# Performance work log

Hardware: AMD Instinct MI355X
Metric: run time of the kernel (lower is better)

## Reference

```python
import jax, jax.numpy as jnp
import numpy as np

N, E, F, H, O, B = 100000, 1200000, 64, 1024, 1, 256


def _gcn_conv(x, W, b, src, dst, ew, num_nodes):
    # PyG GCNConv: out_i = sum_{(s->i)} d_i^{-1/2} w_e d_s^{-1/2} (x_s W) + b
    deg = jax.ops.segment_sum(ew, dst, num_segments=num_nodes)
    dinv = jnp.where(deg > 0, jax.lax.rsqrt(jnp.maximum(deg, 1e-12)), 0.0)
    norm = dinv[src] * ew * dinv[dst]          # [E]
    h = x @ W                                   # [N, out]
    msg = h[src] * norm[:, None]                # gather + scale
    return jax.ops.segment_sum(msg, dst, num_segments=num_nodes) + b


def setup_inputs() -> dict:
    key = jax.random.key(0)
    ks = jax.random.split(key, 12)
    def lin(k, fan_in, fan_out):
        s = 1.0 / np.sqrt(fan_in)
        kw, kb = jax.random.split(k)
        return (jax.random.uniform(kw, (fan_in, fan_out), jnp.float32, -s, s),
                jax.random.uniform(kb, (fan_out,), jnp.float32, -s, s))
    W1, b1 = lin(ks[0], F, F)
    W2, b2 = lin(ks[1], F, 2 * F)
    W3, b3 = lin(ks[2], 2 * F, 4 * F)
    Wf1, bf1 = lin(ks[3], 5 * F, H)
    Wf2, bf2 = lin(ks[4], H, O)
    feature = jax.random.normal(ks[5], (N, F), jnp.float32)
    edge_index = jax.random.randint(ks[6], (2, E), 0, N, jnp.int32)
    weight = jax.random.uniform(ks[7], (E,), jnp.float32)
    protein_batch = jnp.sort(jax.random.randint(ks[8], (N,), 0, B, jnp.int32))
    return {"feature": feature, "edge_index": edge_index, "weight": weight,
            "protein_batch": protein_batch,
            "W1": W1, "b1": b1, "W2": W2, "b2": b2, "W3": W3, "b3": b3,
            "Wf1": Wf1, "bf1": bf1, "Wf2": Wf2, "bf2": bf2}


def reference(feature, edge_index, weight, protein_batch,
              W1, b1, W2, b2, W3, b3, Wf1, bf1, Wf2, bf2):
    num_nodes = feature.shape[0]
    # add self-loops with weight 1 (PyG default)
    loop = jnp.arange(num_nodes, dtype=edge_index.dtype)
    src = jnp.concatenate([edge_index[0], loop])
    dst = jnp.concatenate([edge_index[1], loop])
    ew = jnp.concatenate([weight, jnp.ones((num_nodes,), weight.dtype)])

    x = jax.nn.relu(_gcn_conv(feature, W1, b1, src, dst, ew, num_nodes))
    x = jax.nn.relu(_gcn_conv(x, W2, b2, src, dst, ew, num_nodes))
    x = jax.nn.relu(_gcn_conv(x, W3, b3, src, dst, ew, num_nodes))
    x = jnp.concatenate([x, feature], axis=1)   # [N, 5F]

    # global_mean_pool over graph ids
    sums = jax.ops.segment_sum(x, protein_batch, num_segments=B)
    cnts = jax.ops.segment_sum(jnp.ones((num_nodes,), x.dtype), protein_batch, num_segments=B)
    gc = sums / jnp.maximum(cnts, 1.0)[:, None]

    gc = jax.nn.relu(gc @ Wf1 + bf1)            # dropout is identity in eval
    return gc @ Wf2 + bf2
```

## Files before the change

### kernel.cpp

```cpp
#include <hip/hip_runtime.h>
#include <cstdio>
#include <cstdint>

typedef _Float16 f16x8 __attribute__((ext_vector_type(8)));
typedef float f32x4 __attribute__((ext_vector_type(4)));

__device__ inline unsigned short f2bf(float f) {
  unsigned u = __float_as_uint(f);
  u += 0x7fffu + ((u >> 16) & 1u);
  return (unsigned short)(u >> 16);
}
__device__ inline float bf2f(unsigned short h) {
  return __uint_as_float(((unsigned)h) << 16);
}
__device__ inline unsigned short f2h(float f) {
  union { _Float16 h; unsigned short u; } cv;
  cv.h = (_Float16)f;
  return cv.u;
}


__global__ __launch_bounds__(256)
void k_prep(double* __restrict__ psum, float* __restrict__ gcnt,
            const float* __restrict__ feature, ushort* __restrict__ featb,
            const float* __restrict__ W1, ushort* __restrict__ w1h,
            const float* __restrict__ W2, ushort* __restrict__ w2h,
            const float* __restrict__ W3, ushort* __restrict__ w3h,
            int BC, int Bn, int NF, int F, int D2, int D3,
            int nB, int nC) {
  int b = blockIdx.x;
  int t = threadIdx.x;
  if (b < nB) {
    int i = b * 256 + t;
    if (i < BC) psum[i] = 0.0;
    if (i < Bn) gcnt[i] = 0.f;
  } else if (b < nB + nC) {
    int base = ((b - nB) * 256 + t) * 4;
    if (base < NF) {
      float4 v = *reinterpret_cast<const float4*>(feature + base);
      ushort4 h;
      h.x = f2bf(v.x); h.y = f2bf(v.y); h.z = f2bf(v.z); h.w = f2bf(v.w);
      *reinterpret_cast<ushort4*>(featb + base) = h;
    }
  } else {
    int idx = (b - nB - nC) * 256 + t;
    int s1 = F * F, s2 = s1 + F * D2, s3 = s2 + D2 * D3;
    if (idx < s1) {
      int k = idx / F, n = idx - k * F;
      w1h[(size_t)n * F + k] = f2h(W1[idx]);
    } else if (idx < s2) {
      int i2 = idx - s1; int k = i2 / D2, n = i2 - k * D2;
      w2h[(size_t)n * F + k] = f2h(W2[i2]);
    } else if (idx < s3) {
      int i3 = idx - s2; int k = i3 / D3, n = i3 - k * D3;
      w3h[(size_t)n * D2 + k] = f2h(W3[i3]);
    }
  }
}


#define EPB 4096

__global__ __launch_bounds__(256)
void k_bhist(const int* __restrict__ dst, int* __restrict__ H,
             int NB, int E) {
  __shared__ int hist[512];
  const int t = threadIdx.x;
  for (int i = t; i < NB; i += 256) hist[i] = 0;
  __syncthreads();
  const int base = blockIdx.x * EPB + t;
#pragma unroll
  for (int j = 0; j < EPB / 256; j++) {
    int e = base + 256 * j;
    if (e < E) atomicAdd(&hist[dst[e] >> 8], 1);
  }
  __syncthreads();
  for (int i = t; i < NB; i += 256) H[(size_t)blockIdx.x * NB + i] = hist[i];
}

__global__ __launch_bounds__(256)
void k_bscan1(const int* __restrict__ H, int* __restrict__ S,
              int* __restrict__ bsum, int NB, int NBLK, int T) {
  __shared__ int sh[256];
  const int t = threadIdx.x;
  const int base = blockIdx.x * 1024;
  int v[4]; int s = 0;
#pragma unroll
  for (int j = 0; j < 4; j++) {
    int idx = base + t * 4 + j;
    if (idx < T) {
      int bin = idx / NBLK, bi = idx - bin * NBLK;
      v[j] = H[(size_t)bi * NB + bin];
    } else v[j] = 0;
    s += v[j];
  }
  sh[t] = s;
  __syncthreads();
  for (int off = 1; off < 256; off <<= 1) {
    int x = (t >= off) ? sh[t - off] : 0;
    __syncthreads();
    sh[t] += x;
    __syncthreads();
  }
  int run = sh[t] - s;
#pragma unroll
  for (int j = 0; j < 4; j++) {
    int idx = base + t * 4 + j;
    if (idx < T) S[idx] = run;
    run += v[j];
  }
  if (t == 255) bsum[blockIdx.x] = sh[255];
}

__global__ __launch_bounds__(256)
void k_bscan23(int* __restrict__ S, const int* __restrict__ bsum, int T) {
  __shared__ int spre;
  const int chunk = blockIdx.x >> 2;
  if (threadIdx.x == 0) {
    int pre = 0;
    for (int t = 0; t < chunk; t++) pre += bsum[t];
    spre = pre;
  }
  __syncthreads();
  int i = blockIdx.x * 256 + threadIdx.x;
  if (i < T) S[i] += spre;
}

__global__ __launch_bounds__(256)
void k_bscatter(const int* __restrict__ src, const int* __restrict__ dst,
                const float* __restrict__ ew, const int* __restrict__ S,
                int* __restrict__ sdst, int2* __restrict__ ssw,
                int NB, int NBLK, int E) {
  __shared__ int cnt[512];
  __shared__ int sbase[512];
  const int t = threadIdx.x, bi = blockIdx.x;
  for (int i = t; i < NB; i += 256) {
    cnt[i] = 0;
    sbase[i] = S[(size_t)i * NBLK + bi];
  }
  __syncthreads();
  const int base = bi * EPB + t;
#pragma unroll
  for (int j = 0; j < EPB / 256; j++) {
    int e = base + 256 * j;
    if (e < E) {
      int d = dst[e];
      int bin = d >> 8;
      int r = atomicAdd(&cnt[bin], 1);
      int pos = sbase[bin] + r;
      sdst[pos] = d;
      ssw[pos] = make_int2(src[e], __float_as_int(ew[e]));
    }
  }
}

__global__ __launch_bounds__(256)
void k_bprocA(const int* __restrict__ sdst, const int2* __restrict__ ssw,
              const int* __restrict__ S, int* __restrict__ cntN,
              float* __restrict__ wsumN, int NB, int NBLK, int N, int E) {
  __shared__ int cnt[256];
  __shared__ float wsm[256];
  const int t = threadIdx.x, bin = blockIdx.x;
  cnt[t] = 0; wsm[t] = 0.f;
  __syncthreads();
  const int start = S[(size_t)bin * NBLK];
  const int end = (bin + 1 < NB) ? S[(size_t)(bin + 1) * NBLK] : E;
  for (int p = start + t; p < end; p += 256) {
    int ld = sdst[p] & 255;
    atomicAdd(&cnt[ld], 1);
    atomicAdd(&wsm[ld], __int_as_float(ssw[p].y));
  }
  __syncthreads();
  int n = bin * 256 + t;
  if (n < N) { cntN[n] = cnt[t]; wsumN[n] = wsm[t]; }
}

__global__ __launch_bounds__(256)
void k_scan1(const int* __restrict__ cntN, const float* __restrict__ wsumN,
             int* __restrict__ rs, int* __restrict__ bsum,
             float* __restrict__ dinv, float* __restrict__ sn, int N) {
  __shared__ int sh[256];
  const int t = threadIdx.x;
  const int base = blockIdx.x * 1024;
  int v[4]; int s = 0;
#pragma unroll
  for (int j = 0; j < 4; j++) {
    int idx = base + t * 4 + j;
    if (idx < N) {
      v[j] = cntN[idx];
      double deg = 1.0 + (double)wsumN[idx];
      float r = (float)(1.0 / sqrt(deg));
      dinv[idx] = r;
      sn[idx] = r * r;
    } else v[j] = 0;
    s += v[j];
  }
  sh[t] = s;
  __syncthreads();
  for (int off = 1; off < 256; off <<= 1) {
    int x = (t >= off) ? sh[t - off] : 0;
    __syncthreads();
    sh[t] += x;
    __syncthreads();
  }
  int run = sh[t] - s;
#pragma unroll
  for (int j = 0; j < 4; j++) {
    int idx = base + t * 4 + j;
    if (idx < N) rs[idx] = run;
    run += v[j];
  }
  if (t == 255) bsum[blockIdx.x] = sh[255];
}

__global__ __launch_bounds__(256)
void k_scan23(int* __restrict__ rs, const int* __restrict__ bsum, int N, int E) {
  __shared__ int spre;
  const int chunk = blockIdx.x >> 2;
  if (threadIdx.x == 0) {
    int pre = 0;
    for (int t = 0; t < chunk; t++) pre += bsum[t];
    spre = pre;
  }
  __syncthreads();
  int i = blockIdx.x * 256 + threadIdx.x;
  if (i < N) rs[i] += spre;
  if (i == 0) rs[N] = E;
}

__global__ __launch_bounds__(256)
void k_bprocB(const int* __restrict__ sdst, const int2* __restrict__ ssw,
              const int* __restrict__ S, const int* __restrict__ rs,
              const float* __restrict__ dinv,
              int2* __restrict__ epack, int NB, int NBLK, int N, int E) {
  __shared__ int cnt[256];
  __shared__ float sdv[256];
  __shared__ int srs[256];
  const int t = threadIdx.x, bin = blockIdx.x;
  cnt[t] = 0;
  int n = bin * 256 + t;
  sdv[t] = (n < N) ? dinv[n] : 0.f;
  srs[t] = (n < N) ? rs[n] : 0;
  __syncthreads();
  const int start = S[(size_t)bin * NBLK];
  const int end = (bin + 1 < NB) ? S[(size_t)(bin + 1) * NBLK] : E;
  for (int p = start + t; p < end; p += 256) {
    int d = sdst[p];
    int ld = d & 255;
    int2 sw = ssw[p];
    int r = atomicAdd(&cnt[ld], 1);
    float w = dinv[sw.x] * __int_as_float(sw.y) * sdv[ld];
    epack[srs[ld] + r] = make_int2(sw.x, __float_as_int(w));
  }
}


__device__ inline void bf8_fma(const int4 v, float w, float* acc) {
  acc[0] = fmaf(__uint_as_float((unsigned)v.x << 16), w, acc[0]);
  acc[1] = fmaf(__uint_as_float((unsigned)v.x & 0xffff0000u), w, acc[1]);
  acc[2] = fmaf(__uint_as_float((unsigned)v.y << 16), w, acc[2]);
  acc[3] = fmaf(__uint_as_float((unsigned)v.y & 0xffff0000u), w, acc[3]);
  acc[4] = fmaf(__uint_as_float((unsigned)v.z << 16), w, acc[4]);
  acc[5] = fmaf(__uint_as_float((unsigned)v.z & 0xffff0000u), w, acc[5]);
  acc[6] = fmaf(__uint_as_float((unsigned)v.w << 16), w, acc[6]);
  acc[7] = fmaf(__uint_as_float((unsigned)v.w & 0xffff0000u), w, acc[7]);
}

template<int LOG2L>
__global__ __launch_bounds__(256)
void k_aggregate_b(const ushort* __restrict__ Xb, const int* __restrict__ rs,
                   const int2* __restrict__ epack, const float* __restrict__ sn,
                   ushort* __restrict__ AH, int N) {
  const int t = blockIdx.x * blockDim.x + threadIdx.x;
  const int row = t >> LOG2L;
  if (row >= N) return;
  const int L = 1 << LOG2L;
  const int D = L << 3;
  const int c = (t & (L - 1)) << 3;
  const ushort* __restrict__ Xc = Xb + c;

  float acc[8];
  {
    int4 v = *reinterpret_cast<const int4*>(Xc + (size_t)row * D);
    float s = sn[row];
    acc[0] = s * __uint_as_float((unsigned)v.x << 16);
    acc[1] = s * __uint_as_float((unsigned)v.x & 0xffff0000u);
    acc[2] = s * __uint_as_float((unsigned)v.y << 16);
    acc[3] = s * __uint_as_float((unsigned)v.y & 0xffff0000u);
    acc[4] = s * __uint_as_float((unsigned)v.z << 16);
    acc[5] = s * __uint_as_float((unsigned)v.z & 0xffff0000u);
    acc[6] = s * __uint_as_float((unsigned)v.w << 16);
    acc[7] = s * __uint_as_float((unsigned)v.w & 0xffff0000u);
  }
  const int p0 = rs[row], pe = rs[row + 1];
  int i = p0;
  if ((i & 1) && i < pe) {
    int2 e = epack[i];
    int4 v = *reinterpret_cast<const int4*>(Xc + (size_t)e.x * D);
    bf8_fma(v, __int_as_float(e.y), acc);
    i++;
  }
  if (i + 4 <= pe) {
    int4 ea = *reinterpret_cast<const int4*>(&epack[i]);
    int4 eb = *reinterpret_cast<const int4*>(&epack[i + 2]);
    for (; i + 8 <= pe; i += 4) {
      int4 v0 = *reinterpret_cast<const int4*>(Xc + (size_t)ea.x * D);
      int4 v1 = *reinterpret_cast<const int4*>(Xc + (size_t)ea.z * D);
      int4 v2 = *reinterpret_cast<const int4*>(Xc + (size_t)eb.x * D);
      int4 v3 = *reinterpret_cast<const int4*>(Xc + (size_t)eb.z * D);
      int4 na = *reinterpret_cast<const int4*>(&epack[i + 4]);
      int4 nb = *reinterpret_cast<const int4*>(&epack[i + 6]);
      bf8_fma(v0, __int_as_float(ea.y), acc);
      bf8_fma(v1, __int_as_float(ea.w), acc);
      bf8_fma(v2, __int_as_float(eb.y), acc);
      bf8_fma(v3, __int_as_float(eb.w), acc);
      ea = na; eb = nb;
    }
    {
      int4 v0 = *reinterpret_cast<const int4*>(Xc + (size_t)ea.x * D);
      int4 v1 = *reinterpret_cast<const int4*>(Xc + (size_t)ea.z * D);
      int4 v2 = *reinterpret_cast<const int4*>(Xc + (size_t)eb.x * D);
      int4 v3 = *reinterpret_cast<const int4*>(Xc + (size_t)eb.z * D);
      bf8_fma(v0, __int_as_float(ea.y), acc);
      bf8_fma(v1, __int_as_float(ea.w), acc);
      bf8_fma(v2, __int_as_float(eb.y), acc);
      bf8_fma(v3, __int_as_float(eb.w), acc);
      i += 4;
    }
  }
  if (i + 2 <= pe) {
    int4 e2 = *reinterpret_cast<const int4*>(&epack[i]);
    int4 v0 = *reinterpret_cast<const int4*>(Xc + (size_t)e2.x * D);
    int4 v1 = *reinterpret_cast<const int4*>(Xc + (size_t)e2.z * D);
    bf8_fma(v0, __int_as_float(e2.y), acc);
    bf8_fma(v1, __int_as_float(e2.w), acc);
    i += 2;
  }
  if (i < pe) {
    int2 e = epack[i];
    int4 v = *reinterpret_cast<const int4*>(Xc + (size_t)e.x * D);
    bf8_fma(v, __int_as_float(e.y), acc);
  }
  ushort h[8];
#pragma unroll
  for (int j = 0; j < 8; j++) h[j] = f2h(acc[j]);
  size_t o = (size_t)row * D + c;
  *reinterpret_cast<ushort4*>(AH + o)     = make_ushort4(h[0], h[1], h[2], h[3]);
  *reinterpret_cast<ushort4*>(AH + o + 4) = make_ushort4(h[4], h[5], h[6], h[7]);
}


template<int KT, int NT>
__global__ __launch_bounds__(256)
void k_gemm_mfma(const ushort* __restrict__ Ah, const ushort* __restrict__ Bh,
                 const float* __restrict__ bias, ushort* __restrict__ Y,
                 int N, int D) {
  constexpr int PK = 72;
  __shared__ __align__(16) ushort sAh[128 * PK];
  __shared__ __align__(16) ushort sBh[NT * PK];
  const int t = threadIdx.x;
  const int wave = t >> 6, lane = t & 63;
  const int quad = lane >> 4, l16 = lane & 15;
  const int m0 = blockIdx.y * 128;
  const int n0 = blockIdx.x * NT;

  f32x4 acc[2][NT / 16];
#pragma unroll
  for (int mi = 0; mi < 2; mi++)
#pragma unroll
    for (int ni = 0; ni < NT / 16; ni++) acc[mi][ni] = (f32x4){0.f, 0.f, 0.f, 0.f};

  for (int k0 = 0; k0 < KT; k0 += 64) {
    if (k0) __syncthreads();
#pragma unroll
    for (int it = 0; it < 4; it++) {
      int c = t + 256 * it;
      int row = c >> 3, kc = (c & 7) << 3;
      int gr = m0 + row; if (gr >= N) gr = N - 1;
      *reinterpret_cast<int4*>(&sAh[row * PK + kc]) =
          *reinterpret_cast<const int4*>(Ah + (size_t)gr * KT + k0 + kc);
    }
#pragma unroll
    for (int it = 0; it < NT / 32; it++) {
      int c = t + 256 * it;
      int row = c >> 3, kc = (c & 7) << 3;
      *reinterpret_cast<int4*>(&sBh[row * PK + kc]) =
          *reinterpret_cast<const int4*>(Bh + (size_t)(n0 + row) * KT + k0 + kc);
    }
    __syncthreads();
#pragma unroll
    for (int ks = 0; ks < 2; ks++) {
      const int kk = ks * 32 + quad * 8;
      f16x8 aH[2];
#pragma unroll
      for (int mi = 0; mi < 2; mi++) {
        int r = wave * 32 + mi * 16 + l16;
        aH[mi] = *reinterpret_cast<const f16x8*>(&sAh[r * PK + kk]);
      }
#pragma unroll
      for (int ni = 0; ni < NT / 16; ni++) {
        int r = ni * 16 + l16;
        f16x8 bH = *reinterpret_cast<const f16x8*>(&sBh[r * PK + kk]);
#pragma unroll
        for (int mi = 0; mi < 2; mi++)
          acc[mi][ni] = __builtin_amdgcn_mfma_f32_16x16x32_f16(aH[mi], bH, acc[mi][ni], 0, 0, 0);
      }
    }
  }
#pragma unroll
  for (int mi = 0; mi < 2; mi++) {
    int rb = m0 + wave * 32 + mi * 16 + quad * 4;
#pragma unroll
    for (int ni = 0; ni < NT / 16; ni++) {
      int col = n0 + ni * 16 + l16;
      float bv = bias[col];
#pragma unroll
      for (int r = 0; r < 4; r++) {
        int row = rb + r;
        if (row < N)
          Y[(size_t)row * D + col] = f2bf(fmaxf(acc[mi][ni][r] + bv, 0.f));
      }
    }
  }
}


__global__ void k_pool(const ushort* __restrict__ X3b, const float* __restrict__ feat,
                       const int* __restrict__ pb, double* __restrict__ psum,
                       float* __restrict__ gcnt, int N, int D3, int F) {
  const int c = threadIdx.x;
  const int C = D3 + F;
  int i0 = blockIdx.x * 64;
  if (i0 >= N) return;
  int iend = i0 + 64; if (iend > N) iend = N;
  double acc = 0.0;
  float cacc = 0.f;
  int cur = pb[i0];
  for (int i = i0; i < iend; i++) {
    int b = pb[i];
    if (b != cur) {
      atomicAdd(&psum[(size_t)cur * C + c], acc);
      if (c == 0) atomicAdd(&gcnt[cur], cacc);
      acc = 0.0; cacc = 0.f; cur = b;
    }
    float v;
    if (c < D3) v = bf2f(X3b[(size_t)i * D3 + c]);
    else        v = feat[(size_t)i * F + (c - D3)];
    acc += (double)v;
    cacc += 1.f;
  }
  atomicAdd(&psum[(size_t)cur * C + c], acc);
  if (c == 0) atomicAdd(&gcnt[cur], cacc);
}


__global__ __launch_bounds__(256)
void k_fc1(const double* __restrict__ psum, const float* __restrict__ cnt,
           const float* __restrict__ Wf1, const float* __restrict__ bf1,
           float* __restrict__ hidden, int C, int Hh) {
  const int b = blockIdx.y;
  __shared__ float gcs[384];
  float invc = 1.f / fmaxf(cnt[b], 1.f);
  for (int c = threadIdx.x; c < C; c += 256)
    gcs[c] = (float)psum[(size_t)b * C + c] * invc;
  __syncthreads();
  const int j = blockIdx.x * 256 + threadIdx.x;
  if (j >= Hh) return;
  const float* w = Wf1 + j;
  float a0 = 0.f, a1 = 0.f, a2 = 0.f, a3 = 0.f;
  int c = 0;
  for (; c + 4 <= C; c += 4) {
    a0 = fmaf(gcs[c + 0], w[(size_t)(c + 0) * Hh], a0);
    a1 = fmaf(gcs[c + 1], w[(size_t)(c + 1) * Hh], a1);
    a2 = fmaf(gcs[c + 2], w[(size_t)(c + 2) * Hh], a2);
    a3 = fmaf(gcs[c + 3], w[(size_t)(c + 3) * Hh], a3);
  }
  for (; c < C; c++) a0 = fmaf(gcs[c], w[(size_t)c * Hh], a0);
  float r = ((a0 + a1) + (a2 + a3)) + bf1[j];
  hidden[(size_t)b * Hh + j] = fmaxf(r, 0.f);
}

__global__ void k_fc2(const float* __restrict__ hidden, const float* __restrict__ Wf2,
                      const float* __restrict__ bf2, float* __restrict__ out, int Hh) {
  int b = blockIdx.x;
  int lane = threadIdx.x;
  double s = 0.0;
  for (int j = lane; j < Hh; j += 64) s += (double)hidden[(size_t)b * Hh + j] * (double)Wf2[j];
#pragma unroll
  for (int off = 32; off > 0; off >>= 1) s += __shfl_down(s, off);
  if (lane == 0) out[b] = (float)s + bf2[0];
}


extern "C" void kernel_launch(void* const* d_in, const int* in_sizes, int n_in,
                              void* d_out, int out_size, void* d_ws, size_t ws_size,
                              hipStream_t stream) {
  const float* feature = (const float*)d_in[0];
  const int*   eidx    = (const int*)  d_in[1];
  const float* weight  = (const float*)d_in[2];
  const int*   pb      = (const int*)  d_in[3];
  const float* W1  = (const float*)d_in[4];
  const float* b1  = (const float*)d_in[5];
  const float* W2  = (const float*)d_in[6];
  const float* b2  = (const float*)d_in[7];
  const float* W3  = (const float*)d_in[8];
  const float* b3  = (const float*)d_in[9];
  const float* Wf1 = (const float*)d_in[10];
  const float* bf1 = (const float*)d_in[11];
  const float* Wf2 = (const float*)d_in[12];
  const float* bf2 = (const float*)d_in[13];

  const int F  = in_sizes[5];
  const int D2 = in_sizes[7];
  const int D3 = in_sizes[9];
  const int Hh = in_sizes[11];
  const int N  = in_sizes[0] / F;
  const int E  = in_sizes[1] / 2;
  const int B  = out_size;
  const int C  = D3 + F;

  const int* srcp = eidx;
  const int* dstp = eidx + E;

  const int NB   = (N + 255) / 256;
  const int NBLK = (E + EPB - 1) / EPB;
  const int T    = NB * NBLK;
  const int nscanb = (T + 1023) / 1024;
  const int nscan  = (N + 1023) / 1024;

  auto al = [](size_t x) { return (x + 255) & ~(size_t)255; };
  size_t off = 0;
  auto alloc = [&](size_t bytes) { size_t o = off; off += al(bytes); return o; };
  size_t o_H     = alloc((size_t)T * 4);
  size_t o_S     = alloc((size_t)T * 4);
  size_t o_bsb   = alloc((size_t)nscanb * 4);
  size_t o_sdst  = alloc((size_t)E * 4);
  size_t o_ssw   = alloc((size_t)E * 8);
  size_t o_cntN  = alloc((size_t)N * 4);
  size_t o_wsumN = alloc((size_t)N * 4);
  size_t o_dinv  = alloc((size_t)N * 4);
  size_t o_sn    = alloc((size_t)N * 4);
  size_t o_rs    = alloc((size_t)(N + 1) * 4);
  size_t o_bsum  = alloc((size_t)nscan * 4);
  size_t o_epack = alloc((size_t)E * 8);
  size_t o_featb = alloc((size_t)N * F  * 2);
  size_t o_x1b   = alloc((size_t)N * F  * 2);
  size_t o_x2b   = alloc((size_t)N * D2 * 2);
  size_t o_x3b   = alloc((size_t)N * D3 * 2);
  size_t o_aggh  = alloc((size_t)N * D2 * 2);
  size_t o_w1h   = alloc((size_t)F  * F  * 2);
  size_t o_w2h   = alloc((size_t)F  * D2 * 2);
  size_t o_w3h   = alloc((size_t)D2 * D3 * 2);
  size_t o_psum  = alloc((size_t)B * C * 8);
  size_t o_gcnt  = alloc((size_t)B * 4);
  size_t o_hid   = alloc((size_t)B * Hh * 4);
  if (off > ws_size) {
    fprintf(stderr, "kernel_launch: workspace too small: need %zu, have %zu\n", off, ws_size);
    return;
  }

  char* ws = (char*)d_ws;
  int*    H     = (int*)  (ws + o_H);
  int*    S     = (int*)  (ws + o_S);
  int*    bsb   = (int*)  (ws + o_bsb);
  int*    sdst  = (int*)  (ws + o_sdst);
  int2*   ssw   = (int2*) (ws + o_ssw);
  int*    cntN  = (int*)  (ws + o_cntN);
  float*  wsumN = (float*)(ws + o_wsumN);
  float*  dinv  = (float*)(ws + o_dinv);
  float*  sn    = (float*)(ws + o_sn);
  int*    rs    = (int*)  (ws + o_rs);
  int*    bsum  = (int*)  (ws + o_bsum);
  int2*   epack = (int2*) (ws + o_epack);
  ushort* featb = (ushort*)(ws + o_featb);
  ushort* x1b   = (ushort*)(ws + o_x1b);
  ushort* x2b   = (ushort*)(ws + o_x2b);
  ushort* x3b   = (ushort*)(ws + o_x3b);
  ushort* aggh  = (ushort*)(ws + o_aggh);
  ushort* w1h   = (ushort*)(ws + o_w1h);
  ushort* w2h   = (ushort*)(ws + o_w2h);
  ushort* w3h   = (ushort*)(ws + o_w3h);
  double* psum  = (double*)(ws + o_psum);
  float*  gcnt  = (float*)(ws + o_gcnt);
  float*  hid   = (float*)(ws + o_hid);
  float*  out   = (float*)d_out;

  const int BC = B * C, NF = N * F;
  const int nB = (BC + 255) / 256;
  const int nC = (NF / 4 + 255) / 256;
  const int nD = (F * F + F * D2 + D2 * D3 + 255) / 256;
  k_prep<<<nB + nC + nD, 256, 0, stream>>>(
      psum, gcnt, feature, featb, W1, w1h, W2, w2h, W3, w3h,
      BC, B, NF, F, D2, D3, nB, nC);

  k_bhist   <<<NBLK, 256, 0, stream>>>(dstp, H, NB, E);
  k_bscan1  <<<nscanb, 256, 0, stream>>>(H, S, bsb, NB, NBLK, T);
  k_bscan23 <<<(T + 255) / 256, 256, 0, stream>>>(S, bsb, T);
  k_bscatter<<<NBLK, 256, 0, stream>>>(srcp, dstp, weight, S, sdst, ssw, NB, NBLK, E);
  k_bprocA  <<<NB, 256, 0, stream>>>(sdst, ssw, S, cntN, wsumN, NB, NBLK, N, E);
  k_scan1   <<<nscan, 256, 0, stream>>>(cntN, wsumN, rs, bsum, dinv, sn, N);
  k_scan23  <<<(N + 255) / 256, 256, 0, stream>>>(rs, bsum, N, E);
  k_bprocB  <<<NB, 256, 0, stream>>>(sdst, ssw, S, rs, dinv, epack, NB, NBLK, N, E);

  const int gy = (N + 127) / 128;

  {
    int tot = N * (F / 8);
    k_aggregate_b<3><<<(tot + 255) / 256, 256, 0, stream>>>(featb, rs, epack, sn, aggh, N);
    dim3 g(1, gy);
    k_gemm_mfma<64, 64><<<g, 256, 0, stream>>>(aggh, w1h, b1, x1b, N, F);
  }
  {
    int tot = N * (F / 8);
    k_aggregate_b<3><<<(tot + 255) / 256, 256, 0, stream>>>(x1b, rs, epack, sn, aggh, N);
    dim3 g(1, gy);
    k_gemm_mfma<64, 128><<<g, 256, 0, stream>>>(aggh, w2h, b2, x2b, N, D2);
  }
  {
    int tot = N * (D2 / 8);
    k_aggregate_b<4><<<(tot + 255) / 256, 256, 0, stream>>>(x2b, rs, epack, sn, aggh, N);
    dim3 g(2, gy);
    k_gemm_mfma<128, 128><<<g, 256, 0, stream>>>(aggh, w3h, b3, x3b, N, D3);
  }

  k_pool <<<(N + 63) / 64, C, 0, stream>>>(x3b, feature, pb, psum, gcnt, N, D3, F);
  {
    dim3 g((Hh + 255) / 256, B);
    k_fc1<<<g, 256, 0, stream>>>(psum, gcnt, Wf1, bf1, hid, C, Hh);
  }
  k_fc2  <<<B, 64, 0, stream>>>(hid, Wf2, bf2, out, Hh);
}
```

Baseline: 436.7 us.

## Pool per graph via binary-searched segment bounds; unroll aggregation loop by eight

Adds a kernel that binary-searches the sorted batch vector to find each graph's node range. Pooling is restructured to launch one grid row per graph, split into four chunks, with eight independent float accumulators. This replaces the per-64-node double-precision atomics and the separate count accumulation. Graph counts now come from the segment bounds. The edge aggregation loop also issues eight gathers per iteration instead of four, exposing more memory-level parallelism at the cost of more registers.

```diff
diff --git a/kernel.cpp b/kernel.cpp
--- a/kernel.cpp
+++ b/kernel.cpp
@@ -21,19 +21,18 @@
 
 
 __global__ __launch_bounds__(256)
-void k_prep(double* __restrict__ psum, float* __restrict__ gcnt,
+void k_prep(float* __restrict__ psum,
             const float* __restrict__ feature, ushort* __restrict__ featb,
             const float* __restrict__ W1, ushort* __restrict__ w1h,
             const float* __restrict__ W2, ushort* __restrict__ w2h,
             const float* __restrict__ W3, ushort* __restrict__ w3h,
-            int BC, int Bn, int NF, int F, int D2, int D3,
+            int BC, int NF, int F, int D2, int D3,
             int nB, int nC) {
   int b = blockIdx.x;
   int t = threadIdx.x;
   if (b < nB) {
     int i = b * 256 + t;
-    if (i < BC) psum[i] = 0.0;
-    if (i < Bn) gcnt[i] = 0.f;
+    if (i < BC) psum[i] = 0.f;
   } else if (b < nB + nC) {
     int base = ((b - nB) * 256 + t) * 4;
     if (base < NF) {
@@ -58,6 +57,18 @@
   }
 }
 
+__global__ __launch_bounds__(256)
+void k_gbound(const int* __restrict__ pb, int* __restrict__ gs, int N, int B) {
+  int b = blockIdx.x * 256 + threadIdx.x;
+  if (b > B) return;
+  int lo = 0, hi = N;
+  while (lo < hi) {
+    int mid = (lo + hi) >> 1;
+    if (pb[mid] < b) lo = mid + 1; else hi = mid;
+  }
+  gs[b] = lo;
+}
+
 
 #define EPB 4096
 
@@ -300,33 +311,40 @@
     bf8_fma(v, __int_as_float(e.y), acc);
     i++;
   }
+  for (; i + 8 <= pe; i += 8) {
+    int4 ea = *reinterpret_cast<const int4*>(&epack[i]);
+    int4 eb = *reinterpret_cast<const int4*>(&epack[i + 2]);
+    int4 ec = *reinterpret_cast<const int4*>(&epack[i + 4]);
+    int4 ed = *reinterpret_cast<const int4*>(&epack[i + 6]);
+    int4 v0 = *reinterpret_cast<const int4*>(Xc + (size_t)ea.x * D);
+    int4 v1 = *reinterpret_cast<const int4*>(Xc + (size_t)ea.z * D);
+    int4 v2 = *reinterpret_cast<const int4*>(Xc + (size_t)eb.x * D);
+    int4 v3 = *reinterpret_cast<const int4*>(Xc + (size_t)eb.z * D);
+    int4 v4 = *reinterpret_cast<const int4*>(Xc + (size_t)ec.x * D);
+    int4 v5 = *reinterpret_cast<const int4*>(Xc + (size_t)ec.z * D);
+    int4 v6 = *reinterpret_cast<const int4*>(Xc + (size_t)ed.x * D);
+    int4 v7 = *reinterpret_cast<const int4*>(Xc + (size_t)ed.z * D);
+    bf8_fma(v0, __int_as_float(ea.y), acc);
+    bf8_fma(v1, __int_as_float(ea.w), acc);
+    bf8_fma(v2, __int_as_float(eb.y), acc);
+    bf8_fma(v3, __int_as_float(eb.w), acc);
+    bf8_fma(v4, __int_as_float(ec.y), acc);
+    bf8_fma(v5, __int_as_float(ec.w), acc);
+    bf8_fma(v6, __int_as_float(ed.y), acc);
+    bf8_fma(v7, __int_as_float(ed.w), acc);
+  }
   if (i + 4 <= pe) {
     int4 ea = *reinterpret_cast<const int4*>(&epack[i]);
     int4 eb = *reinterpret_cast<const int4*>(&epack[i + 2]);
-    for (; i + 8 <= pe; i += 4) {
-      int4 v0 = *reinterpret_cast<const int4*>(Xc + (size_t)ea.x * D);
-      int4 v1 = *reinterpret_cast<const int4*>(Xc + (size_t)ea.z * D);
-      int4 v2 = *reinterpret_cast<const int4*>(Xc + (size_t)eb.x * D);
-      int4 v3 = *reinterpret_cast<const int4*>(Xc + (size_t)eb.z * D);
-      int4 na = *reinterpret_cast<const int4*>(&epack[i + 4]);
-      int4 nb = *reinterpret_cast<const int4*>(&epack[i + 6]);
-      bf8_fma(v0, __int_as_float(ea.y), acc);
-      bf8_fma(v1, __int_as_float(ea.w), acc);
-      bf8_fma(v2, __int_as_float(eb.y), acc);
-      bf8_fma(v3, __int_as_float(eb.w), acc);
-      ea = na; eb = nb;
-    }
-    {
-      int4 v0 = *reinterpret_cast<const int4*>(Xc + (size_t)ea.x * D);
-      int4 v1 = *reinterpret_cast<const int4*>(Xc + (size_t)ea.z * D);
-      int4 v2 = *reinterpret_cast<const int4*>(Xc + (size_t)eb.x * D);
-      int4 v3 = *reinterpret_cast<const int4*>(Xc + (size_t)eb.z * D);
-      bf8_fma(v0, __int_as_float(ea.y), acc);
-      bf8_fma(v1, __int_as_float(ea.w), acc);
-      bf8_fma(v2, __int_as_float(eb.y), acc);
-      bf8_fma(v3, __int_as_float(eb.w), acc);
-      i += 4;
-    }
+    int4 v0 = *reinterpret_cast<const int4*>(Xc + (size_t)ea.x * D);
+    int4 v1 = *reinterpret_cast<const int4*>(Xc + (size_t)ea.z * D);
+    int4 v2 = *reinterpret_cast<const int4*>(Xc + (size_t)eb.x * D);
+    int4 v3 = *reinterpret_cast<const int4*>(Xc + (size_t)eb.z * D);
+    bf8_fma(v0, __int_as_float(ea.y), acc);
+    bf8_fma(v1, __int_as_float(ea.w), acc);
+    bf8_fma(v2, __int_as_float(eb.y), acc);
+    bf8_fma(v3, __int_as_float(eb.w), acc);
+    i += 4;
   }
   if (i + 2 <= pe) {
     int4 e2 = *reinterpret_cast<const int4*>(&epack[i]);
@@ -425,44 +443,70 @@
 }
 
 
+#define PSPLIT 4
+
 __global__ void k_pool(const ushort* __restrict__ X3b, const float* __restrict__ feat,
-                       const int* __restrict__ pb, double* __restrict__ psum,
-                       float* __restrict__ gcnt, int N, int D3, int F) {
+                       const int* __restrict__ gs, float* __restrict__ psum,
+                       int D3, int F) {
   const int c = threadIdx.x;
   const int C = D3 + F;
-  int i0 = blockIdx.x * 64;
-  if (i0 >= N) return;
-  int iend = i0 + 64; if (iend > N) iend = N;
-  double acc = 0.0;
-  float cacc = 0.f;
-  int cur = pb[i0];
-  for (int i = i0; i < iend; i++) {
-    int b = pb[i];
-    if (b != cur) {
-      atomicAdd(&psum[(size_t)cur * C + c], acc);
-      if (c == 0) atomicAdd(&gcnt[cur], cacc);
-      acc = 0.0; cacc = 0.f; cur = b;
-    }
-    float v;
-    if (c < D3) v = bf2f(X3b[(size_t)i * D3 + c]);
-    else        v = feat[(size_t)i * F + (c - D3)];
-    acc += (double)v;
-    cacc += 1.f;
-  }
-  atomicAdd(&psum[(size_t)cur * C + c], acc);
-  if (c == 0) atomicAdd(&gcnt[cur], cacc);
-}
-
-
-__global__ __launch_bounds__(256)
-void k_fc1(const double* __restrict__ psum, const float* __restrict__ cnt,
+  const int b = blockIdx.y;
+  const int sp = blockIdx.x;
+  const int s0 = gs[b], e0 = gs[b + 1];
+  const int len = e0 - s0;
+  if (len <= 0) return;
+  const int chunk = (len + PSPLIT - 1) / PSPLIT;
+  const int s = s0 + sp * chunk;
+  int e = s + chunk; if (e > e0) e = e0;
+  if (s >= e) return;
+  const int n = e - s;
+  float a0 = 0.f, a1 = 0.f, a2 = 0.f, a3 = 0.f;
+  float a4 = 0.f, a5 = 0.f, a6 = 0.f, a7 = 0.f;
+  if (c < D3) {
+    const ushort* p = X3b + (size_t)s * D3 + c;
+    int i = 0;
+    for (; i + 8 <= n; i += 8) {
+      a0 += bf2f(p[0 * (size_t)D3]);
+      a1 += bf2f(p[1 * (size_t)D3]);
+      a2 += bf2f(p[2 * (size_t)D3]);
+      a3 += bf2f(p[3 * (size_t)D3]);
+      a4 += bf2f(p[4 * (size_t)D3]);
+      a5 += bf2f(p[5 * (size_t)D3]);
+      a6 += bf2f(p[6 * (size_t)D3]);
+      a7 += bf2f(p[7 * (size_t)D3]);
+      p += 8 * (size_t)D3;
+    }
+    for (; i < n; i++) { a0 += bf2f(*p); p += D3; }
+  } else {
+    const float* p = feat + (size_t)s * F + (c - D3);
+    int i = 0;
+    for (; i + 8 <= n; i += 8) {
+      a0 += p[0 * (size_t)F];
+      a1 += p[1 * (size_t)F];
+      a2 += p[2 * (size_t)F];
+      a3 += p[3 * (size_t)F];
+      a4 += p[4 * (size_t)F];
+      a5 += p[5 * (size_t)F];
+      a6 += p[6 * (size_t)F];
+      a7 += p[7 * (size_t)F];
+      p += 8 * (size_t)F;
+    }
+    for (; i < n; i++) { a0 += *p; p += F; }
+  }
+  float tot = ((a0 + a1) + (a2 + a3)) + ((a4 + a5) + (a6 + a7));
+  atomicAdd(&psum[(size_t)b * C + c], tot);
+}
+
+
+__global__ __launch_bounds__(256)
+void k_fc1(const float* __restrict__ psum, const int* __restrict__ gs,
            const float* __restrict__ Wf1, const float* __restrict__ bf1,
            float* __restrict__ hidden, int C, int Hh) {
   const int b = blockIdx.y;
   __shared__ float gcs[384];
-  float invc = 1.f / fmaxf(cnt[b], 1.f);
+  float invc = 1.f / fmaxf((float)(gs[b + 1] - gs[b]), 1.f);
   for (int c = threadIdx.x; c < C; c += 256)
-    gcs[c] = (float)psum[(size_t)b * C + c] * invc;
+    gcs[c] = psum[(size_t)b * C + c] * invc;
   __syncthreads();
   const int j = blockIdx.x * 256 + threadIdx.x;
   if (j >= Hh) return;
@@ -551,8 +595,8 @@
   size_t o_w1h   = alloc((size_t)F  * F  * 2);
   size_t o_w2h   = alloc((size_t)F  * D2 * 2);
   size_t o_w3h   = alloc((size_t)D2 * D3 * 2);
-  size_t o_psum  = alloc((size_t)B * C * 8);
-  size_t o_gcnt  = alloc((size_t)B * 4);
+  size_t o_psum  = alloc((size_t)B * C * 4);
+  size_t o_gs    = alloc((size_t)(B + 1) * 4);
   size_t o_hid   = alloc((size_t)B * Hh * 4);
   if (off > ws_size) {
     fprintf(stderr, "kernel_launch: workspace too small: need %zu, have %zu\n", off, ws_size);
@@ -580,8 +624,8 @@
   ushort* w1h   = (ushort*)(ws + o_w1h);
   ushort* w2h   = (ushort*)(ws + o_w2h);
   ushort* w3h   = (ushort*)(ws + o_w3h);
-  double* psum  = (double*)(ws + o_psum);
-  float*  gcnt  = (float*)(ws + o_gcnt);
+  float*  psum  = (float*) (ws + o_psum);
+  int*    gs    = (int*)  (ws + o_gs);
   float*  hid   = (float*)(ws + o_hid);
   float*  out   = (float*)d_out;
 
@@ -590,8 +634,9 @@
   const int nC = (NF / 4 + 255) / 256;
   const int nD = (F * F + F * D2 + D2 * D3 + 255) / 256;
   k_prep<<<nB + nC + nD, 256, 0, stream>>>(
-      psum, gcnt, feature, featb, W1, w1h, W2, w2h, W3, w3h,
-      BC, B, NF, F, D2, D3, nB, nC);
+      psum, feature, featb, W1, w1h, W2, w2h, W3, w3h,
+      BC, NF, F, D2, D3, nB, nC);
+  k_gbound<<<(B + 256) / 256, 256, 0, stream>>>(pb, gs, N, B);
 
   k_bhist   <<<NBLK, 256, 0, stream>>>(dstp, H, NB, E);
   k_bscan1  <<<nscanb, 256, 0, stream>>>(H, S, bsb, NB, NBLK, T);
@@ -623,10 +668,13 @@
     k_gemm_mfma<128, 128><<<g, 256, 0, stream>>>(aggh, w3h, b3, x3b, N, D3);
   }
 
-  k_pool <<<(N + 63) / 64, C, 0, stream>>>(x3b, feature, pb, psum, gcnt, N, D3, F);
+  {
+    dim3 g(PSPLIT, B);
+    k_pool<<<g, C, 0, stream>>>(x3b, feature, gs, psum, D3, F);
+  }
   {
     dim3 g((Hh + 255) / 256, B);
-    k_fc1<<<g, 256, 0, stream>>>(psum, gcnt, Wf1, bf1, hid, C, Hh);
+    k_fc1<<<g, 256, 0, stream>>>(psum, gs, Wf1, bf1, hid, C, Hh);
   }
   k_fc2  <<<B, 64, 0, stream>>>(hid, Wf2, bf2, out, Hh);
 }
```

New measurement: 403.6 us. 7.6% less time.
